# Performance work log

Measured on AMD Instinct MI355X. Metric: run time of the kernel, lower is better.

The kernel has to match this reference:

```python
import jax, jax.numpy as jnp
import numpy as np

L, C, K, V, G, T, NC, CIN = 9, 256, 3, 25, 9, 128, 60, 3


def _ln(x, w, b, axes, eps=1e-5):
    # LayerNorm over (channels, joints) per time step, affine params broadcast over time
    m = x.mean(axes, keepdims=True)
    v = x.var(axes, keepdims=True)
    return (x - m) * jax.lax.rsqrt(v + eps) * w + b


def setup_inputs() -> dict:
    key = jax.random.key(0)
    ks = jax.random.split(key, 8)
    s = 0.02  # weight init scale
    return {
        "x": jax.random.normal(ks[0], (1, CIN, T, V), jnp.float32),
        "A": jax.random.uniform(ks[1], (K, V, V), jnp.float32),
        "ln_in_w": jnp.ones((CIN, V), jnp.float32),
        "ln_in_b": jnp.zeros((CIN, V), jnp.float32),
        "W_in": jax.random.normal(ks[2], (C, CIN), jnp.float32) * s,
        "b_in": jnp.zeros((C,), jnp.float32),
        "Wg": jax.random.normal(ks[3], (L, K * C, C), jnp.float32) * s,
        "bg": jnp.zeros((L, K * C), jnp.float32),
        "ln1_w": jnp.ones((L, C, V), jnp.float32),
        "ln1_b": jnp.zeros((L, C, V), jnp.float32),
        "Wt": jax.random.normal(ks[4], (L, C, C, G), jnp.float32) * s,
        "bt": jnp.zeros((L, C), jnp.float32),
        "ln2_w": jnp.ones((L, C, V), jnp.float32),
        "ln2_b": jnp.zeros((L, C, V), jnp.float32),
        "imp": jnp.ones((L, K, V, V), jnp.float32),
        "W_out": jax.random.normal(ks[5], (NC, C), jnp.float32) * s,
        "b_out": jnp.zeros((NC,), jnp.float32),
    }


def reference(x, A, ln_in_w, ln_in_b, W_in, b_in, Wg, bg, ln1_w, ln1_b,
              Wt, bt, ln2_w, ln2_b, imp, W_out, b_out):
    ghalf = G // 2
    Al = A[None] * imp                      # (L, K, V, V) edge-importance weighted adjacency
    xs = x[0].transpose(1, 0, 2)            # (T, CIN, V): stream frames
    fifo0 = jnp.zeros((L, C, G, V), x.dtype)

    def step(carry, xt):
        fifo, fifo_res = carry
        # input LayerNorm + 1x1 conv (fcn_in)
        h = _ln(xt, ln_in_w, ln_in_b, (0, 1))
        h = jnp.einsum('oc,cv->ov', W_in, h) + b_in[:, None]   # (C, V)
        new_f, new_fr = [], []
        for l in range(L):
            res = h                                             # identity residual (in==out, stride==1)
            # graph conv: 1x1 conv -> (K, C, V), einsum with partitioned adjacency
            y = (jnp.einsum('oc,cv->ov', Wg[l], h) + bg[l][:, None]).reshape(K, C, V)
            z = jnp.einsum('kcv,kvw->cw', y, Al[l])             # (C, V)
            # FIFO shift: newest frame at time index 0
            f = jnp.concatenate([z[:, None, :], fifo[l, :, :-1]], axis=1)      # (C, G, V)
            fr = jnp.concatenate([res[:, None, :], fifo_res[l, :, :-1]], axis=1)
            # tcn: LN -> ReLU -> temporal conv (G,1) -> LN
            a = jax.nn.relu(_ln(f, ln1_w[l][:, None, :], ln1_b[l][:, None, :], (0, 2)))
            t = jnp.einsum('ocg,cgv->ov', Wt[l], a) + bt[l][:, None]           # (C, V)
            t = _ln(t, ln2_w[l], ln2_b[l], (0, 1))
            # residual from center of residual FIFO, then ReLU
            h = jax.nn.relu(t + fr[:, ghalf])
            new_f.append(f)
            new_fr.append(fr)
        pooled = h.mean(axis=1)                                 # avg_pool2d over (T=1, V)
        logits = W_out @ pooled + b_out                         # (NC,)
        return (jnp.stack(new_f), jnp.stack(new_fr)), logits

    _, out = jax.lax.scan(step, (fifo0, fifo0), xs)
    return out  # (T, NC): per-frame class logits
```

## Files before the change

### kernel.cpp

```cpp
#include <hip/hip_runtime.h>

#define TT  128
#define CC  256
#define VV  25
#define KK  3
#define GG  9
#define LL  9
#define NCC 60
#define CINN 3
#define TV    (TT*VV)
#define KDIM2 (CC*GG)
#define UR    ((TT+8)*32)
#define YSTR  104
#define HSTR  264

typedef __attribute__((ext_vector_type(8))) short bf16x8;
typedef __attribute__((ext_vector_type(4))) float f32x4;
typedef unsigned short us16;

__device__ __forceinline__ us16 f2bf(float f) {
    union { float f; unsigned u; } a; a.f = f;
    unsigned r = a.u + 0x7fff + ((a.u >> 16) & 1);
    return (us16)(r >> 16);
}
__device__ __forceinline__ bf16x8 ld8(const us16* p) { return *(const bf16x8*)p; }


#define PN1 (LL*KK*CC*CC)
#define PN2 (LL*CC*CC*GG)
#define PN3 (LL*KK*32*32)
#define PN4 (LL*CC*32)
#define PTOT (PN1+PN2+PN3+PN4)

__global__ void k_prep(const float* __restrict__ Wg, const float* __restrict__ Wt,
                       const float* __restrict__ A, const float* __restrict__ imp,
                       const float* __restrict__ bg,
                       us16* __restrict__ Wgb, us16* __restrict__ Wt2b,
                       us16* __restrict__ AlTb, float* __restrict__ bgAl) {
    int i = blockIdx.x * 256 + threadIdx.x;
    if (i < PN1) {
        Wgb[i] = f2bf(Wg[i]);
    } else if (i < PN1 + PN2) {
        int j = i - PN1;
        int kk = j % (CC*GG);
        int o  = (j / (CC*GG)) % CC;
        int l  = j / (CC*CC*GG);
        int g = kk >> 8, c = kk & 255;
        Wt2b[j] = f2bf(Wt[((size_t)(l*CC + o)*CC + c)*GG + g]);
    } else if (i < PN1 + PN2 + PN3) {
        int j = i - PN1 - PN2;
        int v = j & 31, w = (j >> 5) & 31;
        int lk = j >> 10, k = lk % KK, l = lk / KK;
        float val = 0.f;
        if (v < VV && w < VV)
            val = A[(k*VV+v)*VV + w] * imp[((size_t)(l*KK+k)*VV+v)*VV + w];
        AlTb[j] = f2bf(val);
    } else if (i < PTOT) {
        int j = i - PN1 - PN2 - PN3;
        int w = j & 31, c = (j >> 5) & 255, l = j >> 13;
        float s = 0.f;
        if (w < VV) {
            for (int k = 0; k < KK; k++) {
                float col = 0.f;
                for (int v = 0; v < VV; v++)
                    col += A[(k*VV+v)*VV + w] * imp[((size_t)(l*KK+k)*VV+v)*VV + w];
                s += bg[l*KK*CC + k*CC + c] * col;
            }
        }
        bgAl[j] = s;
    }
}


__device__ __forceinline__ void blk_reduce2(float& s, float& q, float* red) {
    #pragma unroll
    for (int off = 32; off; off >>= 1) {
        s += __shfl_down(s, off);
        q += __shfl_down(q, off);
    }
    int lane = threadIdx.x & 63, w = threadIdx.x >> 6;
    if (lane == 0) { red[w] = s; red[4+w] = q; }
    __syncthreads();
    s = red[0]+red[1]+red[2]+red[3];
    q = red[4]+red[5]+red[6]+red[7];
}


template<int FIRST>
__global__ __launch_bounds__(256) void k_gcn(
    const float* __restrict__ x, const float* __restrict__ lniw,
    const float* __restrict__ lnib, const float* __restrict__ Win,
    const float* __restrict__ bin,
    const us16* __restrict__ Wgb, const us16* __restrict__ Hbt2,
    const us16* __restrict__ AlTb, const float* __restrict__ bgAl,
    const float* __restrict__ lnw, const float* __restrict__ lnb,
    float* __restrict__ HT0, us16* __restrict__ Ut2) {

    const int t = blockIdx.x, tid = threadIdx.x;
    if (t >= TT) {
        int tp = t - TT, c = tid;
        #pragma unroll
        for (int w = 0; w < 32; w++) {
            float u = (w < VV) ? fmaxf(lnb[c*VV + w], 0.f) : 0.f;
            Ut2[(size_t)(tp*32 + w)*CC + c] = f2bf(u);
        }
        return;
    }
    __shared__ us16 Yt[CC*YSTR];
    __shared__ us16 sH[FIRST ? 32*HSTR : 4];
    __shared__ float red[8];
    __shared__ float sx[80];
    __shared__ float sh[80];
    const int wave = tid >> 6, lane = tid & 63, quad = lane >> 4, l16 = lane & 15;

    if (FIRST) {
        if (tid < CINN*VV)
            sx[tid] = x[(size_t)(tid/VV)*TV + t*VV + (tid%VV)];
        __syncthreads();
        float s = 0.f, q = 0.f;
        for (int i = 0; i < CINN*VV; i++) { float v = sx[i]; s += v; q += v*v; }
        float m  = s * (1.f/75.f);
        float var = q * (1.f/75.f) - m*m;
        float rs = rsqrtf(var + 1e-5f);
        if (tid < CINN*VV)
            sh[tid] = (sx[tid]-m)*rs*lniw[tid] + lnib[tid];
        __syncthreads();
        int c = tid;
        float w0 = Win[c*3+0], w1 = Win[c*3+1], w2 = Win[c*3+2], bb = bin[c];
        #pragma unroll
        for (int v = 0; v < VV; v++) {
            float acc = bb + w0*sh[v] + w1*sh[VV+v] + w2*sh[2*VV+v];
            HT0[(size_t)(t*32 + v)*CC + c] = acc;
            sH[v*HSTR + c] = f2bf(acc);
        }
        #pragma unroll
        for (int v = VV; v < 32; v++)
            sH[v*HSTR + c] = 0;
        __syncthreads();
    }

    bf16x8 bf[2][8];
    #pragma unroll
    for (int nt = 0; nt < 2; nt++)
        #pragma unroll
        for (int s = 0; s < 8; s++) {
            if (FIRST)
                bf[nt][s] = *(const bf16x8*)(sH + (nt*16 + l16)*HSTR + s*32 + quad*8);
            else
                bf[nt][s] = ld8(Hbt2 + (size_t)(t*32 + nt*16 + l16)*CC + s*32 + quad*8);
        }
    f32x4 acc[12][2];
    #pragma unroll
    for (int mt = 0; mt < 12; mt++) { acc[mt][0] = (f32x4){}; acc[mt][1] = (f32x4){}; }
    #pragma unroll
    for (int mt = 0; mt < 12; mt++) {
        const us16* ap = Wgb + (size_t)(wave*192 + mt*16 + l16)*CC + quad*8;
        #pragma unroll
        for (int s = 0; s < 8; s++) {
            bf16x8 a = ld8(ap + s*32);
            acc[mt][0] = __builtin_amdgcn_mfma_f32_16x16x32_bf16(a, bf[0][s], acc[mt][0], 0,0,0);
            acc[mt][1] = __builtin_amdgcn_mfma_f32_16x16x32_bf16(a, bf[1][s], acc[mt][1], 0,0,0);
        }
    }
    #pragma unroll
    for (int mt = 0; mt < 12; mt++)
        #pragma unroll
        for (int nt = 0; nt < 2; nt++)
            #pragma unroll
            for (int r = 0; r < 4; r++) {
                int m = wave*192 + mt*16 + quad*4 + r;
                Yt[(m & 255)*YSTR + (m >> 8)*32 + nt*16 + l16] = f2bf(acc[mt][nt][r]);
            }
    __syncthreads();

    bf16x8 al[2][3];
    #pragma unroll
    for (int nt = 0; nt < 2; nt++)
        #pragma unroll
        for (int s = 0; s < 3; s++)
            al[nt][s] = ld8(AlTb + (size_t)(s*32 + nt*16 + l16)*32 + quad*8);
    f32x4 z[4][2];
    #pragma unroll
    for (int mt = 0; mt < 4; mt++) { z[mt][0] = (f32x4){}; z[mt][1] = (f32x4){}; }
    #pragma unroll
    for (int mt = 0; mt < 4; mt++)
        #pragma unroll
        for (int s = 0; s < 3; s++) {
            bf16x8 a = *(const bf16x8*)(Yt + (wave*64 + mt*16 + l16)*YSTR + s*32 + quad*8);
            z[mt][0] = __builtin_amdgcn_mfma_f32_16x16x32_bf16(a, al[0][s], z[mt][0], 0,0,0);
            z[mt][1] = __builtin_amdgcn_mfma_f32_16x16x32_bf16(a, al[1][s], z[mt][1], 0,0,0);
        }

    float s_ = 0.f, q_ = 0.f;
    #pragma unroll
    for (int mt = 0; mt < 4; mt++)
        #pragma unroll
        for (int nt = 0; nt < 2; nt++)
            #pragma unroll
            for (int r = 0; r < 4; r++) {
                int c = wave*64 + mt*16 + quad*4 + r;
                int w = nt*16 + l16;
                float zb = z[mt][nt][r] + bgAl[c*32 + w];
                z[mt][nt][r] = zb;
                if (w < VV) { s_ += zb; q_ += zb*zb; }
            }
    blk_reduce2(s_, q_, red);
    float m = s_ * (1.f/6400.f);
    float var = q_ * (1.f/6400.f) - m*m;
    float rs = rsqrtf(var + 1e-5f);
    #pragma unroll
    for (int mt = 0; mt < 4; mt++)
        #pragma unroll
        for (int nt = 0; nt < 2; nt++) {
            int w = nt*16 + l16;
            if (w < VV) {
                int c0 = wave*64 + mt*16 + quad*4;
                ushort4 pk;
                float u0 = fmaxf((z[mt][nt][0]-m)*rs*lnw[(c0+0)*VV+w] + lnb[(c0+0)*VV+w], 0.f);
                float u1 = fmaxf((z[mt][nt][1]-m)*rs*lnw[(c0+1)*VV+w] + lnb[(c0+1)*VV+w], 0.f);
                float u2 = fmaxf((z[mt][nt][2]-m)*rs*lnw[(c0+2)*VV+w] + lnb[(c0+2)*VV+w], 0.f);
                float u3 = fmaxf((z[mt][nt][3]-m)*rs*lnw[(c0+3)*VV+w] + lnb[(c0+3)*VV+w], 0.f);
                pk.x = f2bf(u0); pk.y = f2bf(u1); pk.z = f2bf(u2); pk.w = f2bf(u3);
                *(ushort4*)(Ut2 + (size_t)((t+8)*32 + w)*CC + c0) = pk;
            }
        }
    #pragma unroll
    for (int r = VV; r < 32; r++)
        Ut2[(size_t)((t+8)*32 + r)*CC + tid] = 0;
}


template<int LAST>
__global__ __launch_bounds__(256) void k_tcn(
    const us16* __restrict__ Wt2, const us16* __restrict__ Ut2,
    const float* __restrict__ btv,
    const float* __restrict__ lnw, const float* __restrict__ lnb,
    const float* __restrict__ HprevT, float* __restrict__ HnextT,
    us16* __restrict__ Hbt2,
    const float* __restrict__ Wout, const float* __restrict__ bout,
    float* __restrict__ out) {

    const int t = blockIdx.x, tid = threadIdx.x;
    const int wave = tid >> 6, lane = tid & 63, quad = lane >> 4, l16 = lane & 15;
    __shared__ float red[8];
    __shared__ float so[LAST ? CC*33 : 4];

    f32x4 acc[4][2];
    #pragma unroll
    for (int mt = 0; mt < 4; mt++) { acc[mt][0] = (f32x4){}; acc[mt][1] = (f32x4){}; }

    bf16x8 sa[3][4], sb[3][2];
    const us16* apb = Wt2 + (size_t)(wave*64 + l16)*KDIM2 + quad*8;

    #define LOADSTAGE(st, it) { \
        int k0 = (it)*32; \
        int g = k0 >> 8; \
        const us16* ub = Ut2 + (size_t)((t + 8 - g)*32)*CC + (k0 & 255) + quad*8; \
        sb[st][0] = ld8(ub + (size_t)l16*CC); \
        sb[st][1] = ld8(ub + (size_t)(16 + l16)*CC); \
        _Pragma("unroll") \
        for (int mt = 0; mt < 4; mt++) \
            sa[st][mt] = ld8(apb + (size_t)(mt*16)*KDIM2 + k0); \
    }
    #define MFSTAGE(st) { \
        _Pragma("unroll") \
        for (int mt = 0; mt < 4; mt++) { \
            acc[mt][0] = __builtin_amdgcn_mfma_f32_16x16x32_bf16(sa[st][mt], sb[st][0], acc[mt][0], 0,0,0); \
            acc[mt][1] = __builtin_amdgcn_mfma_f32_16x16x32_bf16(sa[st][mt], sb[st][1], acc[mt][1], 0,0,0); \
        } \
    }

    LOADSTAGE(0, 0); LOADSTAGE(1, 1); LOADSTAGE(2, 2);
    #pragma unroll 3
    for (int it = 3; it < KDIM2/32; it++) {
        int st = it % 3;
        switch (st) {
            case 0: MFSTAGE(0); LOADSTAGE(0, it); break;
            case 1: MFSTAGE(1); LOADSTAGE(1, it); break;
            default: MFSTAGE(2); LOADSTAGE(2, it); break;
        }
    }
    MFSTAGE(0); MFSTAGE(1); MFSTAGE(2);

    float s_ = 0.f, q_ = 0.f;
    #pragma unroll
    for (int mt = 0; mt < 4; mt++)
        #pragma unroll
        for (int nt = 0; nt < 2; nt++)
            #pragma unroll
            for (int r = 0; r < 4; r++) {
                int c = wave*64 + mt*16 + quad*4 + r;
                int v = nt*16 + l16;
                float val = acc[mt][nt][r] + btv[c];
                acc[mt][nt][r] = val;
                if (v < VV) { s_ += val; q_ += val*val; }
            }
    blk_reduce2(s_, q_, red);
    float m = s_ * (1.f/6400.f);
    float var = q_ * (1.f/6400.f) - m*m;
    float rs = rsqrtf(var + 1e-5f);

    #pragma unroll
    for (int mt = 0; mt < 4; mt++)
        #pragma unroll
        for (int nt = 0; nt < 2; nt++) {
            int v = nt*16 + l16;
            if (v < VV) {
                int c0 = wave*64 + mt*16 + quad*4;
                float o[4];
                #pragma unroll
                for (int r = 0; r < 4; r++) {
                    int c = c0 + r;
                    float res = (t >= 4) ? HprevT[(size_t)((t-4)*32 + v)*CC + c] : 0.f;
                    o[r] = fmaxf((acc[mt][nt][r]-m)*rs*lnw[c*VV+v] + lnb[c*VV+v] + res, 0.f);
                }
                if (LAST) {
                    #pragma unroll
                    for (int r = 0; r < 4; r++) so[(c0+r)*33 + v] = o[r];
                } else {
                    float4 fv; fv.x = o[0]; fv.y = o[1]; fv.z = o[2]; fv.w = o[3];
                    *(float4*)(HnextT + (size_t)(t*32 + v)*CC + c0) = fv;
                    ushort4 pk;
                    pk.x = f2bf(o[0]); pk.y = f2bf(o[1]); pk.z = f2bf(o[2]); pk.w = f2bf(o[3]);
                    *(ushort4*)(Hbt2 + (size_t)(t*32 + v)*CC + c0) = pk;
                }
            }
        }
    if (LAST) {
        __syncthreads();
        int c = tid;
        float pool = 0.f;
        #pragma unroll
        for (int v = 0; v < VV; v++) pool += so[c*33 + v];
        so[c*33 + 32] = pool * (1.f/VV);
        __syncthreads();
        if (tid < NCC) {
            float a = bout[tid];
            for (int cc = 0; cc < CC; cc++) a = fmaf(Wout[tid*CC+cc], so[cc*33 + 32], a);
            out[t*NCC + tid] = a;
        }
    } else {
        #pragma unroll
        for (int v = VV; v < 32; v++)
            Hbt2[(size_t)(t*32 + v)*CC + tid] = 0;
    }
}


extern "C" void kernel_launch(void* const* d_in, const int* in_sizes, int n_in,
                              void* d_out, int out_size, void* d_ws, size_t ws_size,
                              hipStream_t stream) {
    const float* x    = (const float*)d_in[0];
    const float* A    = (const float*)d_in[1];
    const float* lniw = (const float*)d_in[2];
    const float* lnib = (const float*)d_in[3];
    const float* Win  = (const float*)d_in[4];
    const float* bin  = (const float*)d_in[5];
    const float* Wg   = (const float*)d_in[6];
    const float* bg   = (const float*)d_in[7];
    const float* ln1w = (const float*)d_in[8];
    const float* ln1b = (const float*)d_in[9];
    const float* Wt   = (const float*)d_in[10];
    const float* bt   = (const float*)d_in[11];
    const float* ln2w = (const float*)d_in[12];
    const float* ln2b = (const float*)d_in[13];
    const float* imp  = (const float*)d_in[14];
    const float* Wout = (const float*)d_in[15];
    const float* bout = (const float*)d_in[16];
    float* out = (float*)d_out;

    float* ws = (float*)d_ws;
    size_t off = 0;
    auto alloc = [&](size_t n) { float* p = ws + off; off += (n + 255) & ~(size_t)255; return p; };
    float* HT0  = alloc((size_t)TT*32*CC);
    float* HT1  = alloc((size_t)TT*32*CC);
    float* bgAl = alloc((size_t)LL*CC*32);
    us16* Wgb  = (us16*)alloc((size_t)LL*KK*CC*CC/2);
    us16* Wt2b = (us16*)alloc((size_t)LL*CC*KDIM2/2);
    us16* Hbt2 = (us16*)alloc((size_t)TT*32*CC/2);
    us16* Ut2  = (us16*)alloc((size_t)UR*CC/2);
    us16* AlTb = (us16*)alloc((size_t)LL*KK*32*32/2);
    (void)ws_size; (void)in_sizes; (void)n_in; (void)out_size;

    k_prep<<<(PTOT + 255)/256, 256, 0, stream>>>(Wg, Wt, A, imp, bg,
                                                 Wgb, Wt2b, AlTb, bgAl);

    float* hPrev = HT0; float* hNext = HT1;
    for (int l = 0; l < LL; l++) {
        if (l == 0)
            k_gcn<1><<<TT + 8, 256, 0, stream>>>(
                x, lniw, lnib, Win, bin,
                Wgb, Hbt2, AlTb, bgAl, ln1w, ln1b, HT0, Ut2);
        else
            k_gcn<0><<<TT + 8, 256, 0, stream>>>(
                x, lniw, lnib, Win, bin,
                Wgb + (size_t)l*KK*CC*CC, Hbt2,
                AlTb + (size_t)l*KK*32*32, bgAl + (size_t)l*CC*32,
                ln1w + (size_t)l*CC*VV, ln1b + (size_t)l*CC*VV, HT0, Ut2);
        if (l < LL-1) {
            k_tcn<0><<<TT, 256, 0, stream>>>(
                Wt2b + (size_t)l*CC*KDIM2, Ut2, bt + (size_t)l*CC,
                ln2w + (size_t)l*CC*VV, ln2b + (size_t)l*CC*VV,
                hPrev, hNext, Hbt2, Wout, bout, out);
            float* tmp = hPrev; hPrev = hNext; hNext = tmp;
        } else {
            k_tcn<1><<<TT, 256, 0, stream>>>(
                Wt2b + (size_t)l*CC*KDIM2, Ut2, bt + (size_t)l*CC,
                ln2w + (size_t)l*CC*VV, ln2b + (size_t)l*CC*VV,
                hPrev, hNext, Hbt2, Wout, bout, out);
        }
    }
}
```

Before: 816.2 us.

## Fuse temporal conv of layer l-1 with graph conv of layer l into one kernel

Merges the tcn kernel of the previous layer with the gcn kernel of the next layer, so each layer needs one launch instead of two and the intermediate h stays in shared memory instead of a global round trip. The residual and hidden activations are stored in bf16 instead of fp32, and the U buffers are double-buffered because the fused kernel reads the previous layer's U while writing the next. The Wg GEMM is rewritten with a three-stage register prefetch pipeline. The change adds rounding error from the bf16 residual, and launch_bounds(256,1) plus a larger shared footprint may lower occupancy.

```diff
diff --git a/kernel.cpp b/kernel.cpp
--- a/kernel.cpp
+++ b/kernel.cpp
@@ -18,10 +18,15 @@
 typedef __attribute__((ext_vector_type(4))) float f32x4;
 typedef unsigned short us16;
 
+#define MFMA __builtin_amdgcn_mfma_f32_16x16x32_bf16
+
 __device__ __forceinline__ us16 f2bf(float f) {
     union { float f; unsigned u; } a; a.f = f;
     unsigned r = a.u + 0x7fff + ((a.u >> 16) & 1);
     return (us16)(r >> 16);
+}
+__device__ __forceinline__ float bf2f(us16 u) {
+    union { unsigned u; float f; } a; a.u = ((unsigned)u) << 16; return a.f;
 }
 __device__ __forceinline__ bf16x8 ld8(const us16* p) { return *(const bf16x8*)p; }
 
@@ -86,15 +91,40 @@
 }
 
 
+#define TLD(S, it) { \
+    int k0_ = (it)*32; \
+    S##a0 = ld8(wp0 + k0_); \
+    S##a1 = ld8(wp0 + (size_t)16*KDIM2 + k0_); \
+    S##a2 = ld8(wp0 + (size_t)32*KDIM2 + k0_); \
+    S##a3 = ld8(wp0 + (size_t)48*KDIM2 + k0_); \
+    int g_ = k0_ >> 8; \
+    const us16* bp_ = Ut2prev + (size_t)((t + 8 - g_)*32 + l16)*CC + (k0_ & 255) + quad*8; \
+    S##b0 = ld8(bp_); \
+    S##b1 = ld8(bp_ + 16*CC); }
+#define TMF(S) { \
+    acc[0][0] = MFMA(S##a0, S##b0, acc[0][0],0,0,0); \
+    acc[0][1] = MFMA(S##a0, S##b1, acc[0][1],0,0,0); \
+    acc[1][0] = MFMA(S##a1, S##b0, acc[1][0],0,0,0); \
+    acc[1][1] = MFMA(S##a1, S##b1, acc[1][1],0,0,0); \
+    acc[2][0] = MFMA(S##a2, S##b0, acc[2][0],0,0,0); \
+    acc[2][1] = MFMA(S##a2, S##b1, acc[2][1],0,0,0); \
+    acc[3][0] = MFMA(S##a3, S##b0, acc[3][0],0,0,0); \
+    acc[3][1] = MFMA(S##a3, S##b1, acc[3][1],0,0,0); }
+
+
 template<int FIRST>
-__global__ __launch_bounds__(256) void k_gcn(
+__global__ __launch_bounds__(256, 1) void k_layer(
     const float* __restrict__ x, const float* __restrict__ lniw,
     const float* __restrict__ lnib, const float* __restrict__ Win,
     const float* __restrict__ bin,
-    const us16* __restrict__ Wgb, const us16* __restrict__ Hbt2,
+    const us16* __restrict__ Wt2, const us16* __restrict__ Ut2prev,
+    const float* __restrict__ btv,
+    const float* __restrict__ ln2w, const float* __restrict__ ln2b,
+    const us16* __restrict__ HresidTb,
+    const us16* __restrict__ Wgb,
     const us16* __restrict__ AlTb, const float* __restrict__ bgAl,
     const float* __restrict__ lnw, const float* __restrict__ lnb,
-    float* __restrict__ HT0, us16* __restrict__ Ut2) {
+    us16* __restrict__ HTb, us16* __restrict__ Ut2next) {
 
     const int t = blockIdx.x, tid = threadIdx.x;
     if (t >= TT) {
@@ -102,12 +132,12 @@
         #pragma unroll
         for (int w = 0; w < 32; w++) {
             float u = (w < VV) ? fmaxf(lnb[c*VV + w], 0.f) : 0.f;
-            Ut2[(size_t)(tp*32 + w)*CC + c] = f2bf(u);
+            Ut2next[(size_t)(tp*32 + w)*CC + c] = f2bf(u);
         }
         return;
     }
-    __shared__ us16 Yt[CC*YSTR];
-    __shared__ us16 sH[FIRST ? 32*HSTR : 4];
+    __shared__ __align__(16) us16 Yt[CC*YSTR];
+    __shared__ __align__(16) us16 sH[32*HSTR];
     __shared__ float red[8];
     __shared__ float sx[80];
     __shared__ float sh[80];
@@ -130,48 +160,73 @@
         #pragma unroll
         for (int v = 0; v < VV; v++) {
             float acc = bb + w0*sh[v] + w1*sh[VV+v] + w2*sh[2*VV+v];
-            HT0[(size_t)(t*32 + v)*CC + c] = acc;
-            sH[v*HSTR + c] = f2bf(acc);
+            us16 b = f2bf(acc);
+            HTb[(size_t)(t*32 + v)*CC + c] = b;
+            sH[v*HSTR + c] = b;
         }
         #pragma unroll
         for (int v = VV; v < 32; v++)
             sH[v*HSTR + c] = 0;
         __syncthreads();
-    }
-
-    bf16x8 bf[2][8];
-    #pragma unroll
-    for (int nt = 0; nt < 2; nt++)
-        #pragma unroll
-        for (int s = 0; s < 8; s++) {
-            if (FIRST)
-                bf[nt][s] = *(const bf16x8*)(sH + (nt*16 + l16)*HSTR + s*32 + quad*8);
-            else
-                bf[nt][s] = ld8(Hbt2 + (size_t)(t*32 + nt*16 + l16)*CC + s*32 + quad*8);
-        }
-    f32x4 acc[12][2];
-    #pragma unroll
-    for (int mt = 0; mt < 12; mt++) { acc[mt][0] = (f32x4){}; acc[mt][1] = (f32x4){}; }
-    #pragma unroll
-    for (int mt = 0; mt < 12; mt++) {
-        const us16* ap = Wgb + (size_t)(wave*192 + mt*16 + l16)*CC + quad*8;
-        #pragma unroll
-        for (int s = 0; s < 8; s++) {
-            bf16x8 a = ld8(ap + s*32);
-            acc[mt][0] = __builtin_amdgcn_mfma_f32_16x16x32_bf16(a, bf[0][s], acc[mt][0], 0,0,0);
-            acc[mt][1] = __builtin_amdgcn_mfma_f32_16x16x32_bf16(a, bf[1][s], acc[mt][1], 0,0,0);
-        }
-    }
-    #pragma unroll
-    for (int mt = 0; mt < 12; mt++)
-        #pragma unroll
-        for (int nt = 0; nt < 2; nt++)
+    } else {
+        f32x4 acc[4][2];
+        #pragma unroll
+        for (int mt = 0; mt < 4; mt++) { acc[mt][0] = (f32x4){}; acc[mt][1] = (f32x4){}; }
+        const us16* wp0 = Wt2 + (size_t)(wave*64 + l16)*KDIM2 + quad*8;
+        bf16x8 tXa0,tXa1,tXa2,tXa3,tXb0,tXb1;
+        bf16x8 tYa0,tYa1,tYa2,tYa3,tYb0,tYb1;
+        bf16x8 tZa0,tZa1,tZa2,tZa3,tZb0,tZb1;
+        TLD(tX, 0); TLD(tY, 1); TLD(tZ, 2);
+        #pragma unroll 1
+        for (int it = 3; it < 72; it += 3) {
+            TMF(tX); TLD(tX, it);
+            TMF(tY); TLD(tY, it + 1);
+            TMF(tZ); TLD(tZ, it + 2);
+        }
+        TMF(tX); TMF(tY); TMF(tZ);
+
+        float s_ = 0.f, q_ = 0.f;
+        #pragma unroll
+        for (int mt = 0; mt < 4; mt++)
             #pragma unroll
-            for (int r = 0; r < 4; r++) {
-                int m = wave*192 + mt*16 + quad*4 + r;
-                Yt[(m & 255)*YSTR + (m >> 8)*32 + nt*16 + l16] = f2bf(acc[mt][nt][r]);
-            }
-    __syncthreads();
+            for (int nt = 0; nt < 2; nt++)
+                #pragma unroll
+                for (int r = 0; r < 4; r++) {
+                    int c = wave*64 + mt*16 + quad*4 + r;
+                    int v = nt*16 + l16;
+                    float val = acc[mt][nt][r] + btv[c];
+                    acc[mt][nt][r] = val;
+                    if (v < VV) { s_ += val; q_ += val*val; }
+                }
+        blk_reduce2(s_, q_, red);
+        float m = s_ * (1.f/6400.f);
+        float var = q_ * (1.f/6400.f) - m*m;
+        float rs = rsqrtf(var + 1e-5f);
+        #pragma unroll
+        for (int mt = 0; mt < 4; mt++)
+            #pragma unroll
+            for (int nt = 0; nt < 2; nt++) {
+                int v = nt*16 + l16;
+                if (v < VV) {
+                    int c0 = wave*64 + mt*16 + quad*4;
+                    ushort4 pk;
+                    float o[4];
+                    #pragma unroll
+                    for (int r = 0; r < 4; r++) {
+                        int c = c0 + r;
+                        float res = (t >= 4) ? bf2f(HresidTb[(size_t)((t-4)*32 + v)*CC + c]) : 0.f;
+                        o[r] = fmaxf((acc[mt][nt][r]-m)*rs*ln2w[c*VV+v] + ln2b[c*VV+v] + res, 0.f);
+                    }
+                    pk.x = f2bf(o[0]); pk.y = f2bf(o[1]); pk.z = f2bf(o[2]); pk.w = f2bf(o[3]);
+                    *(ushort4*)(HTb + (size_t)(t*32 + v)*CC + c0) = pk;
+                    *(ushort4*)(sH + v*HSTR + c0) = pk;
+                }
+            }
+        #pragma unroll
+        for (int v = VV; v < 32; v++)
+            sH[v*HSTR + tid] = 0;
+        __syncthreads();
+    }
 
     bf16x8 al[2][3];
     #pragma unroll
@@ -179,6 +234,63 @@
         #pragma unroll
         for (int s = 0; s < 3; s++)
             al[nt][s] = ld8(AlTb + (size_t)(s*32 + nt*16 + l16)*32 + quad*8);
+
+    bf16x8 bf[2][8];
+    #pragma unroll
+    for (int nt = 0; nt < 2; nt++)
+        #pragma unroll
+        for (int s = 0; s < 8; s++)
+            bf[nt][s] = *(const bf16x8*)(sH + (nt*16 + l16)*HSTR + s*32 + quad*8);
+
+    bf16x8 wA0,wA1,wA2,wA3,wA4,wA5,wA6,wA7;
+    bf16x8 wB0,wB1,wB2,wB3,wB4,wB5,wB6,wB7;
+    bf16x8 wC0,wC1,wC2,wC3,wC4,wC5,wC6,wC7;
+
+#define PLD(S, mtv) { \
+    const us16* ap_ = Wgb + (size_t)(wave*192 + (mtv)*16 + l16)*CC + quad*8; \
+    S##0 = ld8(ap_);       S##1 = ld8(ap_ + 32); \
+    S##2 = ld8(ap_ + 64);  S##3 = ld8(ap_ + 96); \
+    S##4 = ld8(ap_ + 128); S##5 = ld8(ap_ + 160); \
+    S##6 = ld8(ap_ + 192); S##7 = ld8(ap_ + 224); }
+#define PMFW(S, mtv) { \
+    f32x4 p0a = {}, p0b = {}, p1a = {}, p1b = {}; \
+    p0a = MFMA(S##0, bf[0][0], p0a,0,0,0); \
+    p1a = MFMA(S##0, bf[1][0], p1a,0,0,0); \
+    p0b = MFMA(S##1, bf[0][1], p0b,0,0,0); \
+    p1b = MFMA(S##1, bf[1][1], p1b,0,0,0); \
+    p0a = MFMA(S##2, bf[0][2], p0a,0,0,0); \
+    p1a = MFMA(S##2, bf[1][2], p1a,0,0,0); \
+    p0b = MFMA(S##3, bf[0][3], p0b,0,0,0); \
+    p1b = MFMA(S##3, bf[1][3], p1b,0,0,0); \
+    p0a = MFMA(S##4, bf[0][4], p0a,0,0,0); \
+    p1a = MFMA(S##4, bf[1][4], p1a,0,0,0); \
+    p0b = MFMA(S##5, bf[0][5], p0b,0,0,0); \
+    p1b = MFMA(S##5, bf[1][5], p1b,0,0,0); \
+    p0a = MFMA(S##6, bf[0][6], p0a,0,0,0); \
+    p1a = MFMA(S##6, bf[1][6], p1a,0,0,0); \
+    p0b = MFMA(S##7, bf[0][7], p0b,0,0,0); \
+    p1b = MFMA(S##7, bf[1][7], p1b,0,0,0); \
+    int mb_ = wave*192 + (mtv)*16 + quad*4; \
+    _Pragma("unroll") \
+    for (int r_ = 0; r_ < 4; r_++) { \
+        int m_ = mb_ + r_; \
+        int base_ = (m_ & 255)*YSTR + (m_ >> 8)*32 + l16; \
+        Yt[base_]      = f2bf(p0a[r_] + p0b[r_]); \
+        Yt[base_ + 16] = f2bf(p1a[r_] + p1b[r_]); \
+    } }
+
+    PLD(wA, 0); PLD(wB, 1); PLD(wC, 2);
+    #pragma unroll 1
+    for (int mt = 0; mt < 9; mt += 3) {
+        PMFW(wA, mt);     PLD(wA, mt + 3);
+        PMFW(wB, mt + 1); PLD(wB, mt + 4);
+        PMFW(wC, mt + 2); PLD(wC, mt + 5);
+    }
+    PMFW(wA, 9); PMFW(wB, 10); PMFW(wC, 11);
+#undef PLD
+#undef PMFW
+    __syncthreads();
+
     f32x4 z[4][2];
     #pragma unroll
     for (int mt = 0; mt < 4; mt++) { z[mt][0] = (f32x4){}; z[mt][1] = (f32x4){}; }
@@ -187,8 +299,8 @@
         #pragma unroll
         for (int s = 0; s < 3; s++) {
             bf16x8 a = *(const bf16x8*)(Yt + (wave*64 + mt*16 + l16)*YSTR + s*32 + quad*8);
-            z[mt][0] = __builtin_amdgcn_mfma_f32_16x16x32_bf16(a, al[0][s], z[mt][0], 0,0,0);
-            z[mt][1] = __builtin_amdgcn_mfma_f32_16x16x32_bf16(a, al[1][s], z[mt][1], 0,0,0);
+            z[mt][0] = MFMA(a, al[0][s], z[mt][0], 0,0,0);
+            z[mt][1] = MFMA(a, al[1][s], z[mt][1], 0,0,0);
         }
 
     float s_ = 0.f, q_ = 0.f;
@@ -221,66 +333,42 @@
                 float u2 = fmaxf((z[mt][nt][2]-m)*rs*lnw[(c0+2)*VV+w] + lnb[(c0+2)*VV+w], 0.f);
                 float u3 = fmaxf((z[mt][nt][3]-m)*rs*lnw[(c0+3)*VV+w] + lnb[(c0+3)*VV+w], 0.f);
                 pk.x = f2bf(u0); pk.y = f2bf(u1); pk.z = f2bf(u2); pk.w = f2bf(u3);
-                *(ushort4*)(Ut2 + (size_t)((t+8)*32 + w)*CC + c0) = pk;
+                *(ushort4*)(Ut2next + (size_t)((t+8)*32 + w)*CC + c0) = pk;
             }
         }
     #pragma unroll
     for (int r = VV; r < 32; r++)
-        Ut2[(size_t)((t+8)*32 + r)*CC + tid] = 0;
-}
-
-
-template<int LAST>
-__global__ __launch_bounds__(256) void k_tcn(
-    const us16* __restrict__ Wt2, const us16* __restrict__ Ut2,
+        Ut2next[(size_t)((t+8)*32 + r)*CC + tid] = 0;
+}
+
+
+__global__ __launch_bounds__(256, 1) void k_fin(
+    const us16* __restrict__ Wt2, const us16* __restrict__ Ut2prev,
+    const us16* __restrict__ HresidTb,
     const float* __restrict__ btv,
     const float* __restrict__ lnw, const float* __restrict__ lnb,
-    const float* __restrict__ HprevT, float* __restrict__ HnextT,
-    us16* __restrict__ Hbt2,
     const float* __restrict__ Wout, const float* __restrict__ bout,
     float* __restrict__ out) {
-
     const int t = blockIdx.x, tid = threadIdx.x;
     const int wave = tid >> 6, lane = tid & 63, quad = lane >> 4, l16 = lane & 15;
     __shared__ float red[8];
-    __shared__ float so[LAST ? CC*33 : 4];
+    __shared__ float so[CC*33];
 
     f32x4 acc[4][2];
     #pragma unroll
     for (int mt = 0; mt < 4; mt++) { acc[mt][0] = (f32x4){}; acc[mt][1] = (f32x4){}; }
-
-    bf16x8 sa[3][4], sb[3][2];
-    const us16* apb = Wt2 + (size_t)(wave*64 + l16)*KDIM2 + quad*8;
-
-    #define LOADSTAGE(st, it) { \
-        int k0 = (it)*32; \
-        int g = k0 >> 8; \
-        const us16* ub = Ut2 + (size_t)((t + 8 - g)*32)*CC + (k0 & 255) + quad*8; \
-        sb[st][0] = ld8(ub + (size_t)l16*CC); \
-        sb[st][1] = ld8(ub + (size_t)(16 + l16)*CC); \
-        _Pragma("unroll") \
-        for (int mt = 0; mt < 4; mt++) \
-            sa[st][mt] = ld8(apb + (size_t)(mt*16)*KDIM2 + k0); \
-    }
-    #define MFSTAGE(st) { \
-        _Pragma("unroll") \
-        for (int mt = 0; mt < 4; mt++) { \
-            acc[mt][0] = __builtin_amdgcn_mfma_f32_16x16x32_bf16(sa[st][mt], sb[st][0], acc[mt][0], 0,0,0); \
-            acc[mt][1] = __builtin_amdgcn_mfma_f32_16x16x32_bf16(sa[st][mt], sb[st][1], acc[mt][1], 0,0,0); \
-        } \
-    }
-
-    LOADSTAGE(0, 0); LOADSTAGE(1, 1); LOADSTAGE(2, 2);
-    #pragma unroll 3
-    for (int it = 3; it < KDIM2/32; it++) {
-        int st = it % 3;
-        switch (st) {
-            case 0: MFSTAGE(0); LOADSTAGE(0, it); break;
-            case 1: MFSTAGE(1); LOADSTAGE(1, it); break;
-            default: MFSTAGE(2); LOADSTAGE(2, it); break;
-        }
-    }
-    MFSTAGE(0); MFSTAGE(1); MFSTAGE(2);
+    const us16* wp0 = Wt2 + (size_t)(wave*64 + l16)*KDIM2 + quad*8;
+    bf16x8 tXa0,tXa1,tXa2,tXa3,tXb0,tXb1;
+    bf16x8 tYa0,tYa1,tYa2,tYa3,tYb0,tYb1;
+    bf16x8 tZa0,tZa1,tZa2,tZa3,tZb0,tZb1;
+    TLD(tX, 0); TLD(tY, 1); TLD(tZ, 2);
+    #pragma unroll 1
+    for (int it = 3; it < 72; it += 3) {
+        TMF(tX); TLD(tX, it);
+        TMF(tY); TLD(tY, it + 1);
+        TMF(tZ); TLD(tZ, it + 2);
+    }
+    TMF(tX); TMF(tY); TMF(tZ);
 
     float s_ = 0.f, q_ = 0.f;
     #pragma unroll
@@ -299,7 +387,6 @@
     float m = s_ * (1.f/6400.f);
     float var = q_ * (1.f/6400.f) - m*m;
     float rs = rsqrtf(var + 1e-5f);
-
     #pragma unroll
     for (int mt = 0; mt < 4; mt++)
         #pragma unroll
@@ -307,42 +394,25 @@
             int v = nt*16 + l16;
             if (v < VV) {
                 int c0 = wave*64 + mt*16 + quad*4;
-                float o[4];
                 #pragma unroll
                 for (int r = 0; r < 4; r++) {
                     int c = c0 + r;
-                    float res = (t >= 4) ? HprevT[(size_t)((t-4)*32 + v)*CC + c] : 0.f;
-                    o[r] = fmaxf((acc[mt][nt][r]-m)*rs*lnw[c*VV+v] + lnb[c*VV+v] + res, 0.f);
+                    float res = (t >= 4) ? bf2f(HresidTb[(size_t)((t-4)*32 + v)*CC + c]) : 0.f;
+                    so[c*33 + v] = fmaxf((acc[mt][nt][r]-m)*rs*lnw[c*VV+v] + lnb[c*VV+v] + res, 0.f);
                 }
-                if (LAST) {
-                    #pragma unroll
-                    for (int r = 0; r < 4; r++) so[(c0+r)*33 + v] = o[r];
-                } else {
-                    float4 fv; fv.x = o[0]; fv.y = o[1]; fv.z = o[2]; fv.w = o[3];
-                    *(float4*)(HnextT + (size_t)(t*32 + v)*CC + c0) = fv;
-                    ushort4 pk;
-                    pk.x = f2bf(o[0]); pk.y = f2bf(o[1]); pk.z = f2bf(o[2]); pk.w = f2bf(o[3]);
-                    *(ushort4*)(Hbt2 + (size_t)(t*32 + v)*CC + c0) = pk;
-                }
-            }
-        }
-    if (LAST) {
-        __syncthreads();
-        int c = tid;
-        float pool = 0.f;
-        #pragma unroll
-        for (int v = 0; v < VV; v++) pool += so[c*33 + v];
-        so[c*33 + 32] = pool * (1.f/VV);
-        __syncthreads();
-        if (tid < NCC) {
-            float a = bout[tid];
-            for (int cc = 0; cc < CC; cc++) a = fmaf(Wout[tid*CC+cc], so[cc*33 + 32], a);
-            out[t*NCC + tid] = a;
-        }
-    } else {
-        #pragma unroll
-        for (int v = VV; v < 32; v++)
-            Hbt2[(size_t)(t*32 + v)*CC + tid] = 0;
+            }
+        }
+    __syncthreads();
+    int c = tid;
+    float pl = 0.f;
+    #pragma unroll
+    for (int v = 0; v < VV; v++) pl += so[c*33 + v];
+    so[c*33 + 32] = pl * (1.f/VV);
+    __syncthreads();
+    if (tid < NCC) {
+        float a = bout[tid];
+        for (int cc = 0; cc < CC; cc++) a = fmaf(Wout[tid*CC+cc], so[cc*33 + 32], a);
+        out[t*NCC + tid] = a;
     }
 }
 
@@ -372,42 +442,45 @@
     float* ws = (float*)d_ws;
     size_t off = 0;
     auto alloc = [&](size_t n) { float* p = ws + off; off += (n + 255) & ~(size_t)255; return p; };
-    float* HT0  = alloc((size_t)TT*32*CC);
-    float* HT1  = alloc((size_t)TT*32*CC);
     float* bgAl = alloc((size_t)LL*CC*32);
+    us16* HTb0 = (us16*)alloc((size_t)TT*32*CC/2);
+    us16* HTb1 = (us16*)alloc((size_t)TT*32*CC/2);
     us16* Wgb  = (us16*)alloc((size_t)LL*KK*CC*CC/2);
     us16* Wt2b = (us16*)alloc((size_t)LL*CC*KDIM2/2);
-    us16* Hbt2 = (us16*)alloc((size_t)TT*32*CC/2);
-    us16* Ut2  = (us16*)alloc((size_t)UR*CC/2);
+    us16* UtA  = (us16*)alloc((size_t)UR*CC/2);
+    us16* UtB  = (us16*)alloc((size_t)UR*CC/2);
     us16* AlTb = (us16*)alloc((size_t)LL*KK*32*32/2);
     (void)ws_size; (void)in_sizes; (void)n_in; (void)out_size;
 
     k_prep<<<(PTOT + 255)/256, 256, 0, stream>>>(Wg, Wt, A, imp, bg,
                                                  Wgb, Wt2b, AlTb, bgAl);
 
-    float* hPrev = HT0; float* hNext = HT1;
+    us16* hPrev = HTb0; us16* hNext = HTb1;
+    us16* uCur = UtA;  us16* uNxt = UtB;
     for (int l = 0; l < LL; l++) {
-        if (l == 0)
-            k_gcn<1><<<TT + 8, 256, 0, stream>>>(
+        if (l == 0) {
+            k_layer<1><<<TT + 8, 256, 0, stream>>>(
                 x, lniw, lnib, Win, bin,
-                Wgb, Hbt2, AlTb, bgAl, ln1w, ln1b, HT0, Ut2);
-        else
-            k_gcn<0><<<TT + 8, 256, 0, stream>>>(
+                Wt2b, uCur, bt, ln2w, ln2b, hPrev,
+                Wgb, AlTb, bgAl, ln1w, ln1b,
+                hPrev , uCur );
+        } else {
+            k_layer<0><<<TT + 8, 256, 0, stream>>>(
                 x, lniw, lnib, Win, bin,
-                Wgb + (size_t)l*KK*CC*CC, Hbt2,
+                Wt2b + (size_t)(l-1)*CC*KDIM2, uCur,
+                bt + (size_t)(l-1)*CC,
+                ln2w + (size_t)(l-1)*CC*VV, ln2b + (size_t)(l-1)*CC*VV,
+                hPrev ,
+                Wgb + (size_t)l*KK*CC*CC,
                 AlTb + (size_t)l*KK*32*32, bgAl + (size_t)l*CC*32,
-                ln1w + (size_t)l*CC*VV, ln1b + (size_t)l*CC*VV, HT0, Ut2);
-        if (l < LL-1) {
-            k_tcn<0><<<TT, 256, 0, stream>>>(
-                Wt2b + (size_t)l*CC*KDIM2, Ut2, bt + (size_t)l*CC,
-                ln2w + (size_t)l*CC*VV, ln2b + (size_t)l*CC*VV,
-                hPrev, hNext, Hbt2, Wout, bout, out);
-            float* tmp = hPrev; hPrev = hNext; hNext = tmp;
-        } else {
-            k_tcn<1><<<TT, 256, 0, stream>>>(
-                Wt2b + (size_t)l*CC*KDIM2, Ut2, bt + (size_t)l*CC,
-                ln2w + (size_t)l*CC*VV, ln2b + (size_t)l*CC*VV,
-                hPrev, hNext, Hbt2, Wout, bout, out);
-        }
-    }
-}
+                ln1w + (size_t)l*CC*VV, ln1b + (size_t)l*CC*VV,
+                hNext , uNxt );
+            us16* tmp = hPrev; hPrev = hNext; hNext = tmp;
+            us16* ut = uCur; uCur = uNxt; uNxt = ut;
+        }
+    }
+    k_fin<<<TT, 256, 0, stream>>>(
+        Wt2b + (size_t)(LL-1)*CC*KDIM2, uCur, hPrev,
+        bt + (size_t)(LL-1)*CC, ln2w + (size_t)(LL-1)*CC*VV, ln2b + (size_t)(LL-1)*CC*VV,
+        Wout, bout, out);
+}
```

After: 795.5 us. -2.5%, faster.
